# Kernel tuning notes

Measured on AMD Instinct MI355X. Metric: run time of the kernel, lower is better.

## Reference

```python
import jax, jax.numpy as jnp
import numpy as np
from jax import lax

B, H, W, CIN = 32, 64, 64, 128
F, KH, KW = 256, 3, 3
NCLS = 10


def setup_inputs() -> dict:
    key = jax.random.key(0)
    k1, k2, k3, k4 = jax.random.split(key, 4)
    x = jax.random.normal(k1, (B, H, W, CIN), dtype=jnp.float32)
    classes = jax.random.randint(k2, (B, 1), 0, NCLS, dtype=jnp.int32)
    kernel = jax.random.normal(k3, (NCLS, KH, KW, CIN, F), dtype=jnp.float32) * 0.05
    bias = jax.random.normal(k4, (NCLS, F), dtype=jnp.float32) * 0.05
    return {"x": x, "classes": classes, "kernel": kernel, "bias": bias}


def reference(x, classes, kernel, bias):
    # classes: [B,1] -> [B]
    cls = jnp.squeeze(classes, axis=1)
    k_per = kernel[cls]   # [B, KH, KW, CIN, F] per-sample gathered expert kernel
    b_per = bias[cls]     # [B, F]

    def conv_one(xi, ki):
        # xi: [H,W,CIN], ki: [KH,KW,CIN,F]
        y = lax.conv_general_dilated(
            xi[None], ki,
            window_strides=(1, 1),
            padding="SAME",
            rhs_dilation=(1, 1),
            dimension_numbers=("NHWC", "HWIO", "NHWC"),
        )
        return y[0]

    out = jax.vmap(conv_one)(x, k_per)          # [B,H,W,F]
    out = out + b_per[:, None, None, :]
    return out
```

## Files before the change

kernel.cpp:

```cpp
#include <hip/hip_runtime.h>
#include <stdint.h>

#define BATCH 32
#define CINX 128
#define FOUT 256
#define NCLS 10
#define NSTEP 18

typedef __bf16 bf16x8 __attribute__((ext_vector_type(8)));
typedef float f32x4 __attribute__((ext_vector_type(4)));

#define WT_SLAB 32768
#define WT_BYTES ((size_t)NCLS * 9 * WT_SLAB * 2)
#define Z_BYTES 4096
#define X16_BYTES ((size_t)BATCH * 4096 * CINX * 2)
#define WS_NEED (WT_BYTES + Z_BYTES + X16_BYTES)

#define BAR() __builtin_amdgcn_s_barrier()
#define SCHEDBAR() __builtin_amdgcn_sched_barrier(0)
#define VMW4() asm volatile("s_waitcnt vmcnt(4)" ::: "memory")
#define VMW0() asm volatile("s_waitcnt vmcnt(0)" ::: "memory")

__device__ __forceinline__ void gl16(const __bf16* g, __bf16* l) {
    __builtin_amdgcn_global_load_lds(
        (const __attribute__((address_space(1))) void*)g,
        (__attribute__((address_space(3))) void*)l, 16, 0, 0);
}

__global__ __launch_bounds__(256) void prep_all(const float* __restrict__ kin,
                                                __bf16* __restrict__ wt,
                                                const float* __restrict__ x,
                                                __bf16* __restrict__ x16,
                                                __bf16* __restrict__ zbuf) {
    if (blockIdx.x < NCLS * 9) {
        __shared__ __bf16 tile[128 * 260];
        const int slab = blockIdx.x;
        const float* src = kin + (size_t)slab * (CINX * FOUT);
        __bf16* dst = wt + (size_t)slab * WT_SLAB;
        const int t = threadIdx.x;
#pragma unroll
        for (int i = 0; i < 32; ++i) {
            int e4 = t + i * 256;
            int c = e4 >> 6, f4 = e4 & 63;
            f32x4 v = *(const f32x4*)(src + (size_t)e4 * 4);
            __bf16* p = &tile[c * 260 + f4 * 4];
            p[0] = (__bf16)v[0]; p[1] = (__bf16)v[1];
            p[2] = (__bf16)v[2]; p[3] = (__bf16)v[3];
        }
        __syncthreads();
#pragma unroll
        for (int i = 0; i < 16; ++i) {
            int g = t + i * 256;
            int h = g >> 10;
            int u = g & 1023;
            int f = u >> 2, slot = u & 3;
            int cu = slot ^ ((f >> 1) & 3);
            int c0 = h * 32 + cu * 8;
            bf16x8 o;
#pragma unroll
            for (int j = 0; j < 8; ++j) o[j] = tile[(c0 + j) * 260 + f];
            *(bf16x8*)(dst + (size_t)g * 8) = o;
        }
    } else {
        const int bx = blockIdx.x - NCLS * 9;
        const size_t u = (size_t)bx * 256 + threadIdx.x;
        f32x4 a = *(const f32x4*)(x + u * 8);
        f32x4 c = *(const f32x4*)(x + u * 8 + 4);
        bf16x8 o;
#pragma unroll
        for (int j = 0; j < 4; ++j) { o[j] = (__bf16)a[j]; o[4 + j] = (__bf16)c[j]; }
        *(bf16x8*)(x16 + u * 8) = o;
        if (bx == 0 && threadIdx.x < 128) {
            bf16x8 z;
#pragma unroll
            for (int j = 0; j < 8; ++j) z[j] = (__bf16)0.f;
            *(bf16x8*)(zbuf + (size_t)threadIdx.x * 8) = z;
        }
    }
}

__global__ __launch_bounds__(512, 2) void conv_main8(
    const __bf16* __restrict__ xg16, const int* __restrict__ cls_g,
    const __bf16* __restrict__ wt, const float* __restrict__ bias,
    const __bf16* __restrict__ zbuf, float* __restrict__ out) {
    __shared__ __align__(16) __bf16 ldsA[2][2][1024 * 8];
    __shared__ __align__(16) __bf16 ldsB[2][2][1024 * 8];

    const int bid0 = blockIdx.x;
    const int swz  = (bid0 & 7) * 64 + (bid0 >> 3);
    const int b    = swz >> 4;
    const int pt   = swz & 15;
    const int cls  = cls_g[b];
    const int y0   = pt << 2;

    const int tid  = threadIdx.x;
    const int lane = tid & 63;
    const int wid  = tid >> 6;
    const int wm   = wid >> 2;
    const int wn   = wid & 3;
    const int l15  = lane & 15;
    const int l4   = lane >> 4;

    const __bf16* xb   = xg16 + (size_t)b * 4096 * CINX;
    const __bf16* wcls = wt + (size_t)cls * 9 * WT_SLAB;

    int pyA[2], gxA[2], cuoffA[2], uS[2];
#pragma unroll
    for (int i = 0; i < 2; ++i) {
        int u = i * 512 + tid;
        int px = u >> 2, slot = u & 3;
        uS[i] = u;
        pyA[i] = px >> 6;
        gxA[i] = px & 63;
        cuoffA[i] = (slot ^ ((px >> 1) & 3)) * 8;
    }
    int unA[8], unB[4];
#pragma unroll
    for (int mt = 0; mt < 8; ++mt) {
        int px = wm * 128 + mt * 16 + l15;
        unA[mt] = px * 4 + (l4 ^ ((px >> 1) & 3));
    }
#pragma unroll
    for (int nt = 0; nt < 4; ++nt) {
        int f = wn * 64 + nt * 16 + l15;
        unB[nt] = f * 4 + (l4 ^ ((f >> 1) & 3));
    }

    f32x4 acc[8][4];
#pragma unroll
    for (int i = 0; i < 8; ++i)
#pragma unroll
        for (int j = 0; j < 4; ++j)
#pragma unroll
            for (int r = 0; r < 4; ++r) acc[i][j][r] = 0.f;

    auto stage = [&](int s2, int kk) {
        const int p = s2 & 1;
        const int tap = s2 >> 1;
        const int dy = tap / 3 - 1, dx = tap % 3 - 1;
        const int choff = (s2 & 1) * 64 + kk * 32;
#pragma unroll
        for (int i = 0; i < 2; ++i) {
            const int gy = y0 + pyA[i] + dy;
            const int gx = gxA[i] + dx;
            const bool v = ((unsigned)gy < 64u) && ((unsigned)gx < 64u);
            const __bf16* src = v
                ? (xb + ((size_t)(gy * 64 + gx)) * CINX + choff + cuoffA[i])
                : (zbuf + (size_t)(uS[i] & 63) * 8);
            gl16(src, &ldsA[p][kk][(size_t)uS[i] * 8]);
        }
        const __bf16* wsrc = wcls + (size_t)tap * WT_SLAB +
                             (size_t)((s2 & 1) * 2 + kk) * 8192;
#pragma unroll
        for (int i = 0; i < 2; ++i)
            gl16(wsrc + (size_t)uS[i] * 8, &ldsB[p][kk][(size_t)uS[i] * 8]);
    };

    bf16x8 afr[4], bfr[4];
    auto ldB = [&](int p, int kk) {
#pragma unroll
        for (int nt = 0; nt < 4; ++nt)
            bfr[nt] = *(const bf16x8*)&ldsB[p][kk][(size_t)unB[nt] * 8];
    };
    auto ldA = [&](int p, int kk, int mh) {
#pragma unroll
        for (int mt = 0; mt < 4; ++mt)
            afr[mt] = *(const bf16x8*)&ldsA[p][kk][(size_t)unA[mh * 4 + mt] * 8];
    };
    auto mm = [&](int mh) {
        __builtin_amdgcn_s_setprio(1);
#pragma unroll
        for (int mt = 0; mt < 4; ++mt)
#pragma unroll
            for (int nt = 0; nt < 4; ++nt)
                acc[mh * 4 + mt][nt] = __builtin_amdgcn_mfma_f32_16x16x32_bf16(
                    afr[mt], bfr[nt], acc[mh * 4 + mt][nt], 0, 0, 0);
        __builtin_amdgcn_s_setprio(0);
    };

    stage(0, 0);
    stage(0, 1);
    VMW4();
    BAR();
    SCHEDBAR();

    for (int s = 0; s < NSTEP - 1; ++s) {
        const int p = s & 1;
        ldB(p, 0); ldA(p, 0, 0); stage(s + 1, 0);
        mm(0);
        ldA(p, 0, 1);
        VMW4();
        BAR();
        SCHEDBAR();
        mm(1);
        ldB(p, 1); ldA(p, 1, 0); stage(s + 1, 1);
        mm(0);
        ldA(p, 1, 1);
        VMW4();
        BAR();
        SCHEDBAR();
        mm(1);
    }
    ldB(1, 0); ldA(1, 0, 0);
    mm(0);
    ldA(1, 0, 1);
    VMW0();
    BAR();
    SCHEDBAR();
    mm(1);
    ldB(1, 1); ldA(1, 1, 0);
    mm(0);
    ldA(1, 1, 1);
    mm(1);

    float bv[4];
#pragma unroll
    for (int nt = 0; nt < 4; ++nt)
        bv[nt] = bias[cls * FOUT + wn * 64 + nt * 16 + l15];

    float* ob = out + ((size_t)b * 4096 + (size_t)pt * 256) * FOUT;
#pragma unroll
    for (int mt = 0; mt < 8; ++mt) {
#pragma unroll
        for (int r = 0; r < 4; ++r) {
            const int row = wm * 128 + mt * 16 + l4 * 4 + r;
            float* orow = ob + (size_t)row * FOUT;
#pragma unroll
            for (int nt = 0; nt < 4; ++nt)
                orow[wn * 64 + nt * 16 + l15] = acc[mt][nt][r] + bv[nt];
        }
    }
}

__global__ __launch_bounds__(256) void prep_w_fb(const float* __restrict__ kin,
                                                 __bf16* __restrict__ wt) {
    __shared__ __bf16 tile[128 * 260];
    const int slab = blockIdx.x;
    const float* src = kin + (size_t)slab * (CINX * FOUT);
    __bf16* dst = wt + (size_t)slab * (16 * 256 * 8);
    const int t = threadIdx.x;
#pragma unroll
    for (int i = 0; i < 32; ++i) {
        int e4 = t + i * 256;
        int c = e4 >> 6, f4 = e4 & 63;
        f32x4 v = *(const f32x4*)(src + (size_t)e4 * 4);
        __bf16* p = &tile[c * 260 + f4 * 4];
        p[0] = (__bf16)v[0]; p[1] = (__bf16)v[1];
        p[2] = (__bf16)v[2]; p[3] = (__bf16)v[3];
    }
    __syncthreads();
#pragma unroll
    for (int i = 0; i < 16; ++i) {
        int g = t + i * 256;
        int cu = g >> 8, f = g & 255;
        bf16x8 o;
#pragma unroll
        for (int j = 0; j < 8; ++j) o[j] = tile[(cu * 8 + j) * 260 + f];
        *(bf16x8*)(dst + (size_t)g * 8) = o;
    }
}

__global__ __launch_bounds__(512, 2) void conv_fb(
    const float* __restrict__ xg, const int* __restrict__ cls_g,
    const __bf16* __restrict__ wt, const float* __restrict__ bias,
    float* __restrict__ out) {
    __shared__ __align__(16) __bf16 ldsA[2][8 * 256 * 8];
    __shared__ __align__(16) __bf16 ldsB[2][8 * 256 * 8];
    const int bid0 = blockIdx.x;
    const int swz = (bid0 & 7) * 64 + (bid0 >> 3);
    const int b = swz >> 4, pt = swz & 15;
    const int cls = cls_g[b];
    const int y0 = pt << 2;
    const int tid = threadIdx.x, lane = tid & 63, wid = tid >> 6;
    const int wm = wid >> 2, wn = wid & 3, l15 = lane & 15, l4 = lane >> 4;
    const float* xb = xg + (size_t)b * 4096 * CINX;
    const __bf16* wcls = wt + (size_t)cls * 9 * (16 * 256 * 8);
    const int tpx = tid >> 1, tch = (tid & 1) * 32;
    const int py = tpx >> 6, px_ = tpx & 63;
    f32x4 acc[8][4];
#pragma unroll
    for (int i = 0; i < 8; ++i)
#pragma unroll
        for (int j = 0; j < 4; ++j)
#pragma unroll
            for (int r = 0; r < 4; ++r) acc[i][j][r] = 0.f;
    f32x4 va[8];
    auto issueB = [&](int s, int buf) {
        const int tap = s >> 1, chalf = (s & 1) << 6;
        const __bf16* wsrc = wcls + (size_t)tap * (16 * 256 * 8) + chalf * 256;
#pragma unroll
        for (int i = 0; i < 4; ++i) {
            const int u = i * 512 + tid;
            gl16(wsrc + (size_t)u * 8, &ldsB[buf][(size_t)u * 8]);
        }
    };
    auto issueA = [&](int s) {
        const int tap = s >> 1, chalf = (s & 1) << 6;
        const int dy = tap / 3 - 1, dx = tap % 3 - 1;
        const int gy = y0 + py + dy, gx = px_ + dx;
        const bool valid = ((unsigned)gy < 64u) && ((unsigned)gx < 64u);
        const float* src = xb + ((size_t)(gy * 64 + gx)) * CINX + chalf + tch;
        if (valid) {
#pragma unroll
            for (int j2 = 0; j2 < 8; ++j2) va[j2] = *(const f32x4*)(src + j2 * 4);
        } else {
#pragma unroll
            for (int j2 = 0; j2 < 8; ++j2)
#pragma unroll
                for (int q = 0; q < 4; ++q) va[j2][q] = 0.f;
        }
    };
    auto writeA = [&](int buf) {
#pragma unroll
        for (int j = 0; j < 4; ++j) {
            bf16x8 pk;
#pragma unroll
            for (int q = 0; q < 4; ++q) {
                pk[q] = (__bf16)va[2 * j][q];
                pk[4 + q] = (__bf16)va[2 * j + 1][q];
            }
            const int u = ((tid & 1) * 4 + j) * 256 + tpx;
            *(bf16x8*)(&ldsA[buf][(size_t)u * 8]) = pk;
        }
    };
    auto compute = [&](int buf) {
#pragma unroll
        for (int kk = 0; kk < 2; ++kk) {
            const int cu = kk * 4 + l4;
            bf16x8 afr[8], bfr[4];
#pragma unroll
            for (int mt = 0; mt < 8; ++mt)
                afr[mt] = *(const bf16x8*)(
                    &ldsA[buf][(size_t)(cu * 256 + wm * 128 + mt * 16 + l15) * 8]);
#pragma unroll
            for (int nt = 0; nt < 4; ++nt)
                bfr[nt] = *(const bf16x8*)(
                    &ldsB[buf][(size_t)(cu * 256 + wn * 64 + nt * 16 + l15) * 8]);
#pragma unroll
            for (int mt = 0; mt < 8; ++mt)
#pragma unroll
                for (int nt = 0; nt < 4; ++nt)
                    acc[mt][nt] = __builtin_amdgcn_mfma_f32_16x16x32_bf16(
                        afr[mt], bfr[nt], acc[mt][nt], 0, 0, 0);
        }
    };
    issueB(0, 0);
    issueA(0);
    writeA(0);
    __syncthreads();
    int cur = 0;
    for (int s = 0; s < NSTEP - 1; ++s) {
        issueB(s + 1, cur ^ 1);
        issueA(s + 1);
        compute(cur);
        writeA(cur ^ 1);
        __syncthreads();
        cur ^= 1;
    }
    compute(cur);
    float bv[4];
#pragma unroll
    for (int nt = 0; nt < 4; ++nt)
        bv[nt] = bias[cls * FOUT + wn * 64 + nt * 16 + l15];
    float* ob = out + ((size_t)b * 4096 + (size_t)pt * 256) * FOUT;
#pragma unroll
    for (int mt = 0; mt < 8; ++mt) {
#pragma unroll
        for (int r = 0; r < 4; ++r) {
            const int row = wm * 128 + mt * 16 + l4 * 4 + r;
            float* orow = ob + (size_t)row * FOUT;
#pragma unroll
            for (int nt = 0; nt < 4; ++nt)
                orow[wn * 64 + nt * 16 + l15] = acc[mt][nt][r] + bv[nt];
        }
    }
}

extern "C" void kernel_launch(void* const* d_in, const int* in_sizes, int n_in,
                              void* d_out, int out_size, void* d_ws, size_t ws_size,
                              hipStream_t stream) {
    const float* x       = (const float*)d_in[0];
    const int*   classes = (const int*)d_in[1];
    const float* kin     = (const float*)d_in[2];
    const float* bias    = (const float*)d_in[3];
    float* out = (float*)d_out;

    char* ws = (char*)d_ws;
    __bf16* wt   = (__bf16*)ws;
    __bf16* zbuf = (__bf16*)(ws + WT_BYTES);
    __bf16* x16  = (__bf16*)(ws + WT_BYTES + Z_BYTES);

    if (ws_size >= WS_NEED) {
        prep_all<<<dim3(NCLS * 9 + 8192), dim3(256), 0, stream>>>(kin, wt, x,
                                                                  x16, zbuf);
        conv_main8<<<dim3(512), dim3(512), 0, stream>>>(x16, classes, wt, bias,
                                                        zbuf, out);
    } else {
        prep_w_fb<<<dim3(NCLS * 9), dim3(256), 0, stream>>>(kin, wt);
        conv_fb<<<dim3(512), dim3(512), 0, stream>>>(x, classes, wt, bias, out);
    }
}
```

Measured before the change: 101.7 us.

## Split conv tiles over output features and shrink LDS for higher occupancy

The main conv kernel now gives each block half of the 256 output features, so there are 1024 blocks, each with a 256x128 tile and 4x4 accumulators per wave instead of 8x4. LDS staging is cut to a 32-channel slice per step, double-buffered over 36 steps, and launch bounds request 4 blocks per CU. The aim is more resident waves to hide load latency and a better spread across CUs. The cost is that every input pixel tile is loaded twice (once per feature half), the pipeline has more, shorter steps and more barriers, and each wave gets less data reuse.

```diff
diff --git a/kernel.cpp b/kernel.cpp
--- a/kernel.cpp
+++ b/kernel.cpp
@@ -5,7 +5,7 @@
 #define CINX 128
 #define FOUT 256
 #define NCLS 10
-#define NSTEP 18
+#define NSTEP36 36
 
 typedef __bf16 bf16x8 __attribute__((ext_vector_type(8)));
 typedef float f32x4 __attribute__((ext_vector_type(4)));
@@ -18,7 +18,8 @@
 
 #define BAR() __builtin_amdgcn_s_barrier()
 #define SCHEDBAR() __builtin_amdgcn_sched_barrier(0)
-#define VMW4() asm volatile("s_waitcnt vmcnt(4)" ::: "memory")
+#define LGKM0() asm volatile("s_waitcnt lgkmcnt(0)" ::: "memory")
+#define VMW3() asm volatile("s_waitcnt vmcnt(3)" ::: "memory")
 #define VMW0() asm volatile("s_waitcnt vmcnt(0)" ::: "memory")
 
 __device__ __forceinline__ void gl16(const __bf16* g, __bf16* l) {
@@ -51,11 +52,11 @@
 #pragma unroll
         for (int i = 0; i < 16; ++i) {
             int g = t + i * 256;
-            int h = g >> 10;
+            int c32 = g >> 10;
             int u = g & 1023;
             int f = u >> 2, slot = u & 3;
             int cu = slot ^ ((f >> 1) & 3);
-            int c0 = h * 32 + cu * 8;
+            int c0 = c32 * 32 + cu * 8;
             bf16x8 o;
 #pragma unroll
             for (int j = 0; j < 8; ++j) o[j] = tile[(c0 + j) * 260 + f];
@@ -79,151 +80,140 @@
     }
 }
 
-__global__ __launch_bounds__(512, 2) void conv_main8(
+__global__ __launch_bounds__(512, 4) void conv_hi(
     const __bf16* __restrict__ xg16, const int* __restrict__ cls_g,
     const __bf16* __restrict__ wt, const float* __restrict__ bias,
     const __bf16* __restrict__ zbuf, float* __restrict__ out) {
-    __shared__ __align__(16) __bf16 ldsA[2][2][1024 * 8];
-    __shared__ __align__(16) __bf16 ldsB[2][2][1024 * 8];
+    __shared__ __align__(16) __bf16 ldsA[2][256 * 32];
+    __shared__ __align__(16) __bf16 ldsB[2][128 * 32];
 
     const int bid0 = blockIdx.x;
-    const int swz  = (bid0 & 7) * 64 + (bid0 >> 3);
-    const int b    = swz >> 4;
-    const int pt   = swz & 15;
+    const int swz  = (bid0 & 7) * 128 + (bid0 >> 3);
+    const int b    = swz >> 5;
+    const int pt   = (swz >> 1) & 15;
+    const int ft   = swz & 1;
     const int cls  = cls_g[b];
     const int y0   = pt << 2;
 
     const int tid  = threadIdx.x;
     const int lane = tid & 63;
     const int wid  = tid >> 6;
-    const int wm   = wid >> 2;
-    const int wn   = wid & 3;
+    const int wm   = wid >> 1;
+    const int wn   = wid & 1;
     const int l15  = lane & 15;
     const int l4   = lane >> 4;
 
     const __bf16* xb   = xg16 + (size_t)b * 4096 * CINX;
     const __bf16* wcls = wt + (size_t)cls * 9 * WT_SLAB;
 
-    int pyA[2], gxA[2], cuoffA[2], uS[2];
+    int pyA[2], gxA[2], cuoffA[2];
 #pragma unroll
     for (int i = 0; i < 2; ++i) {
         int u = i * 512 + tid;
         int px = u >> 2, slot = u & 3;
-        uS[i] = u;
         pyA[i] = px >> 6;
         gxA[i] = px & 63;
         cuoffA[i] = (slot ^ ((px >> 1) & 3)) * 8;
     }
-    int unA[8], unB[4];
-#pragma unroll
-    for (int mt = 0; mt < 8; ++mt) {
-        int px = wm * 128 + mt * 16 + l15;
-        unA[mt] = px * 4 + (l4 ^ ((px >> 1) & 3));
-    }
-#pragma unroll
-    for (int nt = 0; nt < 4; ++nt) {
-        int f = wn * 64 + nt * 16 + l15;
-        unB[nt] = f * 4 + (l4 ^ ((f >> 1) & 3));
-    }
-
-    f32x4 acc[8][4];
-#pragma unroll
-    for (int i = 0; i < 8; ++i)
+    const int swq = (l15 >> 1) & 3;
+    int unA[4], unB[4];
+#pragma unroll
+    for (int mt = 0; mt < 4; ++mt)
+        unA[mt] = (wm * 64 + mt * 16 + l15) * 4 + (l4 ^ swq);
+#pragma unroll
+    for (int nt = 0; nt < 4; ++nt)
+        unB[nt] = (wn * 64 + nt * 16 + l15) * 4 + (l4 ^ swq);
+
+    f32x4 acc[4][4];
+#pragma unroll
+    for (int i = 0; i < 4; ++i)
 #pragma unroll
         for (int j = 0; j < 4; ++j)
 #pragma unroll
             for (int r = 0; r < 4; ++r) acc[i][j][r] = 0.f;
 
-    auto stage = [&](int s2, int kk) {
-        const int p = s2 & 1;
-        const int tap = s2 >> 1;
+    auto stage = [&](int s2, int buf) {
+        const int tap = s2 >> 2, c32 = s2 & 3;
         const int dy = tap / 3 - 1, dx = tap % 3 - 1;
-        const int choff = (s2 & 1) * 64 + kk * 32;
+        const int choff = c32 * 32;
 #pragma unroll
         for (int i = 0; i < 2; ++i) {
+            const int u = i * 512 + tid;
             const int gy = y0 + pyA[i] + dy;
             const int gx = gxA[i] + dx;
             const bool v = ((unsigned)gy < 64u) && ((unsigned)gx < 64u);
             const __bf16* src = v
                 ? (xb + ((size_t)(gy * 64 + gx)) * CINX + choff + cuoffA[i])
-                : (zbuf + (size_t)(uS[i] & 63) * 8);
-            gl16(src, &ldsA[p][kk][(size_t)uS[i] * 8]);
+                : (zbuf + (size_t)(u & 63) * 8);
+            gl16(src, &ldsA[buf][(size_t)u * 8]);
         }
         const __bf16* wsrc = wcls + (size_t)tap * WT_SLAB +
-                             (size_t)((s2 & 1) * 2 + kk) * 8192;
-#pragma unroll
-        for (int i = 0; i < 2; ++i)
-            gl16(wsrc + (size_t)uS[i] * 8, &ldsB[p][kk][(size_t)uS[i] * 8]);
+                             (size_t)(c32 * 1024 + ft * 512 + tid) * 8;
+        gl16(wsrc, &ldsB[buf][(size_t)tid * 8]);
     };
 
     bf16x8 afr[4], bfr[4];
-    auto ldB = [&](int p, int kk) {
+    auto rdfrags = [&](int buf) {
+#pragma unroll
+        for (int mt = 0; mt < 4; ++mt)
+            afr[mt] = *(const bf16x8*)&ldsA[buf][(size_t)unA[mt] * 8];
 #pragma unroll
         for (int nt = 0; nt < 4; ++nt)
-            bfr[nt] = *(const bf16x8*)&ldsB[p][kk][(size_t)unB[nt] * 8];
-    };
-    auto ldA = [&](int p, int kk, int mh) {
+            bfr[nt] = *(const bf16x8*)&ldsB[buf][(size_t)unB[nt] * 8];
+    };
+    auto mm = [&]() {
+        __builtin_amdgcn_s_setprio(1);
 #pragma unroll
         for (int mt = 0; mt < 4; ++mt)
-            afr[mt] = *(const bf16x8*)&ldsA[p][kk][(size_t)unA[mh * 4 + mt] * 8];
-    };
-    auto mm = [&](int mh) {
-        __builtin_amdgcn_s_setprio(1);
-#pragma unroll
-        for (int mt = 0; mt < 4; ++mt)
 #pragma unroll
             for (int nt = 0; nt < 4; ++nt)
-                acc[mh * 4 + mt][nt] = __builtin_amdgcn_mfma_f32_16x16x32_bf16(
-                    afr[mt], bfr[nt], acc[mh * 4 + mt][nt], 0, 0, 0);
+                acc[mt][nt] = __builtin_amdgcn_mfma_f32_16x16x32_bf16(
+                    afr[mt], bfr[nt], acc[mt][nt], 0, 0, 0);
         __builtin_amdgcn_s_setprio(0);
     };
 
     stage(0, 0);
-    stage(0, 1);
-    VMW4();
+    stage(1, 1);
+    VMW3();
     BAR();
+
+    for (int s = 0; s < NSTEP36 - 2; s += 2) {
+#pragma unroll
+        for (int half = 0; half < 2; ++half) {
+            const int buf = half;
+            rdfrags(buf);
+            LGKM0();
+            SCHEDBAR();
+            BAR();
+            stage(s + half + 2, buf);
+            mm();
+            VMW3();
+            BAR();
+        }
+    }
+    rdfrags(0);
+    LGKM0();
     SCHEDBAR();
-
-    for (int s = 0; s < NSTEP - 1; ++s) {
-        const int p = s & 1;
-        ldB(p, 0); ldA(p, 0, 0); stage(s + 1, 0);
-        mm(0);
-        ldA(p, 0, 1);
-        VMW4();
-        BAR();
-        SCHEDBAR();
-        mm(1);
-        ldB(p, 1); ldA(p, 1, 0); stage(s + 1, 1);
-        mm(0);
-        ldA(p, 1, 1);
-        VMW4();
-        BAR();
-        SCHEDBAR();
-        mm(1);
-    }
-    ldB(1, 0); ldA(1, 0, 0);
-    mm(0);
-    ldA(1, 0, 1);
+    BAR();
+    mm();
     VMW0();
     BAR();
+    rdfrags(1);
+    LGKM0();
     SCHEDBAR();
-    mm(1);
-    ldB(1, 1); ldA(1, 1, 0);
-    mm(0);
-    ldA(1, 1, 1);
-    mm(1);
+    mm();
 
     float bv[4];
 #pragma unroll
     for (int nt = 0; nt < 4; ++nt)
-        bv[nt] = bias[cls * FOUT + wn * 64 + nt * 16 + l15];
-
-    float* ob = out + ((size_t)b * 4096 + (size_t)pt * 256) * FOUT;
-#pragma unroll
-    for (int mt = 0; mt < 8; ++mt) {
+        bv[nt] = bias[cls * FOUT + ft * 128 + wn * 64 + nt * 16 + l15];
+
+    float* ob = out + ((size_t)b * 4096 + (size_t)pt * 256) * FOUT + ft * 128;
+#pragma unroll
+    for (int mt = 0; mt < 4; ++mt) {
 #pragma unroll
         for (int r = 0; r < 4; ++r) {
-            const int row = wm * 128 + mt * 16 + l4 * 4 + r;
+            const int row = wm * 64 + mt * 16 + l4 * 4 + r;
             float* orow = ob + (size_t)row * FOUT;
 #pragma unroll
             for (int nt = 0; nt < 4; ++nt)
@@ -349,7 +339,7 @@
     writeA(0);
     __syncthreads();
     int cur = 0;
-    for (int s = 0; s < NSTEP - 1; ++s) {
+    for (int s = 0; s < 17; ++s) {
         issueB(s + 1, cur ^ 1);
         issueA(s + 1);
         compute(cur);
@@ -393,8 +383,8 @@
     if (ws_size >= WS_NEED) {
         prep_all<<<dim3(NCLS * 9 + 8192), dim3(256), 0, stream>>>(kin, wt, x,
                                                                   x16, zbuf);
-        conv_main8<<<dim3(512), dim3(512), 0, stream>>>(x16, classes, wt, bias,
-                                                        zbuf, out);
+        conv_hi<<<dim3(1024), dim3(512), 0, stream>>>(x16, classes, wt, bias,
+                                                      zbuf, out);
     } else {
         prep_w_fb<<<dim3(NCLS * 9), dim3(256), 0, stream>>>(kin, wt);
         conv_fb<<<dim3(512), dim3(512), 0, stream>>>(x, classes, wt, bias, out);
```

Result: slower. 104.4 us (+2.6%).

## Switch conv main loop to 32x32x16 MFMA with double-buffered register fragments

Applied to the files above, without the earlier changes.

Replaces the 16x16x32 bf16 MFMA tiling with 32x32x16 tiles (4x2 per wave instead of 8x4), so fewer LDS fragment reads are needed per FLOP. It adds ping-pong register fragment sets so LDS reads for the next k-step overlap the current MFMAs. It also precomputes per-thread source pointers and a per-tap validity bitmask to cut address arithmetic in the staging loop, and fully unrolls the main loop. The risks are higher register pressure under the 2-blocks-per-SM launch bound, and a more complex output row mapping.

```diff
diff --git a/kernel.cpp b/kernel.cpp
--- a/kernel.cpp
+++ b/kernel.cpp
@@ -5,10 +5,10 @@
 #define CINX 128
 #define FOUT 256
 #define NCLS 10
-#define NSTEP 18
 
 typedef __bf16 bf16x8 __attribute__((ext_vector_type(8)));
 typedef float f32x4 __attribute__((ext_vector_type(4)));
+typedef float f32x16 __attribute__((ext_vector_type(16)));
 
 #define WT_SLAB 32768
 #define WT_BYTES ((size_t)NCLS * 9 * WT_SLAB * 2)
@@ -21,7 +21,7 @@
 #define VMW4() asm volatile("s_waitcnt vmcnt(4)" ::: "memory")
 #define VMW0() asm volatile("s_waitcnt vmcnt(0)" ::: "memory")
 
-__device__ __forceinline__ void gl16(const __bf16* g, __bf16* l) {
+__device__ __forceinline__ void gl16(const void* g, void* l) {
     __builtin_amdgcn_global_load_lds(
         (const __attribute__((address_space(1))) void*)g,
         (__attribute__((address_space(3))) void*)l, 16, 0, 0);
@@ -51,11 +51,11 @@
 #pragma unroll
         for (int i = 0; i < 16; ++i) {
             int g = t + i * 256;
-            int h = g >> 10;
+            int c32 = g >> 10;
             int u = g & 1023;
             int f = u >> 2, slot = u & 3;
             int cu = slot ^ ((f >> 1) & 3);
-            int c0 = h * 32 + cu * 8;
+            int c0 = c32 * 32 + cu * 8;
             bf16x8 o;
 #pragma unroll
             for (int j = 0; j < 8; ++j) o[j] = tile[(c0 + j) * 260 + f];
@@ -79,12 +79,11 @@
     }
 }
 
-__global__ __launch_bounds__(512, 2) void conv_main8(
+__global__ __launch_bounds__(512, 2) void conv32(
     const __bf16* __restrict__ xg16, const int* __restrict__ cls_g,
     const __bf16* __restrict__ wt, const float* __restrict__ bias,
     const __bf16* __restrict__ zbuf, float* __restrict__ out) {
-    __shared__ __align__(16) __bf16 ldsA[2][2][1024 * 8];
-    __shared__ __align__(16) __bf16 ldsB[2][2][1024 * 8];
+    __shared__ __align__(16) char lds[131072];
 
     const int bid0 = blockIdx.x;
     const int swz  = (bid0 & 7) * 64 + (bid0 >> 3);
@@ -98,83 +97,99 @@
     const int wid  = tid >> 6;
     const int wm   = wid >> 2;
     const int wn   = wid & 3;
-    const int l15  = lane & 15;
-    const int l4   = lane >> 4;
+    const int l31  = lane & 31;
+    const int hi   = lane >> 5;
 
     const __bf16* xb   = xg16 + (size_t)b * 4096 * CINX;
     const __bf16* wcls = wt + (size_t)cls * 9 * WT_SLAB;
 
-    int pyA[2], gxA[2], cuoffA[2], uS[2];
+    const __bf16* PA[2];
+    const __bf16* WB[2];
+    const __bf16* ZS[2];
+    int vmask[2];
+    int dstu[2];
 #pragma unroll
     for (int i = 0; i < 2; ++i) {
-        int u = i * 512 + tid;
-        int px = u >> 2, slot = u & 3;
-        uS[i] = u;
-        pyA[i] = px >> 6;
-        gxA[i] = px & 63;
-        cuoffA[i] = (slot ^ ((px >> 1) & 3)) * 8;
-    }
-    int unA[8], unB[4];
-#pragma unroll
-    for (int mt = 0; mt < 8; ++mt) {
-        int px = wm * 128 + mt * 16 + l15;
-        unA[mt] = px * 4 + (l4 ^ ((px >> 1) & 3));
-    }
-#pragma unroll
-    for (int nt = 0; nt < 4; ++nt) {
-        int f = wn * 64 + nt * 16 + l15;
-        unB[nt] = f * 4 + (l4 ^ ((f >> 1) & 3));
-    }
-
-    f32x4 acc[8][4];
-#pragma unroll
-    for (int i = 0; i < 8; ++i)
-#pragma unroll
-        for (int j = 0; j < 4; ++j)
-#pragma unroll
-            for (int r = 0; r < 4; ++r) acc[i][j][r] = 0.f;
+        const int u = i * 512 + tid;
+        const int px = u >> 2, slot = u & 3;
+        const int py = px >> 6, gx = px & 63;
+        const int cuoff = (slot ^ ((px >> 1) & 3)) * 8;
+        const int ay = y0 + py;
+        PA[i] = xb + ((size_t)(ay * 64 + gx)) * CINX + cuoff;
+        WB[i] = wcls + (size_t)u * 8;
+        ZS[i] = zbuf + (size_t)(u & 63) * 8;
+        dstu[i] = u * 16;
+        int m = 0;
+#pragma unroll
+        for (int tap = 0; tap < 9; ++tap) {
+            const int dy = tap / 3 - 1, dx = tap % 3 - 1;
+            const int yy = ay + dy, xx = gx + dx;
+            if (true) m |= ((((unsigned)yy < 64u) && ((unsigned)xx < 64u)) ? 1 : 0) << tap;
+        }
+        vmask[i] = m;
+    }
+
+    int adA[2][4], adB[2][2];
+#pragma unroll
+    for (int mt = 0; mt < 4; ++mt) {
+        const int px = wm * 128 + mt * 32 + l31;
+        const int sw = (px >> 1) & 3;
+#pragma unroll
+        for (int ks = 0; ks < 2; ++ks)
+            adA[ks][mt] = (px * 4 + ((2 * ks + hi) ^ sw)) * 16;
+    }
+#pragma unroll
+    for (int nt = 0; nt < 2; ++nt) {
+        const int f = wn * 64 + nt * 32 + l31;
+        const int sw = (f >> 1) & 3;
+#pragma unroll
+        for (int ks = 0; ks < 2; ++ks)
+            adB[ks][nt] = 65536 + (f * 4 + ((2 * ks + hi) ^ sw)) * 16;
+    }
+
+    f32x16 acc[4][2];
+#pragma unroll
+    for (int i = 0; i < 4; ++i)
+#pragma unroll
+        for (int j = 0; j < 2; ++j)
+#pragma unroll
+            for (int r = 0; r < 16; ++r) acc[i][j][r] = 0.f;
 
     auto stage = [&](int s2, int kk) {
-        const int p = s2 & 1;
+        const int pk  = (s2 & 1) * 2 + kk;
         const int tap = s2 >> 1;
         const int dy = tap / 3 - 1, dx = tap % 3 - 1;
-        const int choff = (s2 & 1) * 64 + kk * 32;
+        const int cq = (s2 & 1) * 2 + kk;
+        const int aoff = (dy * 64 + dx) * CINX + cq * 32;
+        const size_t woff = (size_t)tap * WT_SLAB + (size_t)cq * 8192;
 #pragma unroll
         for (int i = 0; i < 2; ++i) {
-            const int gy = y0 + pyA[i] + dy;
-            const int gx = gxA[i] + dx;
-            const bool v = ((unsigned)gy < 64u) && ((unsigned)gx < 64u);
-            const __bf16* src = v
-                ? (xb + ((size_t)(gy * 64 + gx)) * CINX + choff + cuoffA[i])
-                : (zbuf + (size_t)(uS[i] & 63) * 8);
-            gl16(src, &ldsA[p][kk][(size_t)uS[i] * 8]);
-        }
-        const __bf16* wsrc = wcls + (size_t)tap * WT_SLAB +
-                             (size_t)((s2 & 1) * 2 + kk) * 8192;
+            const __bf16* src = ((vmask[i] >> tap) & 1) ? (PA[i] + aoff) : ZS[i];
+            gl16(src, lds + pk * 16384 + dstu[i]);
+        }
 #pragma unroll
         for (int i = 0; i < 2; ++i)
-            gl16(wsrc + (size_t)uS[i] * 8, &ldsB[p][kk][(size_t)uS[i] * 8]);
-    };
-
-    bf16x8 afr[4], bfr[4];
-    auto ldB = [&](int p, int kk) {
-#pragma unroll
-        for (int nt = 0; nt < 4; ++nt)
-            bfr[nt] = *(const bf16x8*)&ldsB[p][kk][(size_t)unB[nt] * 8];
-    };
-    auto ldA = [&](int p, int kk, int mh) {
+            gl16(WB[i] + woff, lds + 65536 + pk * 16384 + dstu[i]);
+    };
+
+    bf16x8 AS[2][4], BS[2][2];
+    auto rd = [&](int set, int pk, int ks) {
+        const int off = pk * 16384;
 #pragma unroll
         for (int mt = 0; mt < 4; ++mt)
-            afr[mt] = *(const bf16x8*)&ldsA[p][kk][(size_t)unA[mh * 4 + mt] * 8];
-    };
-    auto mm = [&](int mh) {
+            AS[set][mt] = *(const bf16x8*)(lds + off + adA[ks][mt]);
+#pragma unroll
+        for (int nt = 0; nt < 2; ++nt)
+            BS[set][nt] = *(const bf16x8*)(lds + off + adB[ks][nt]);
+    };
+    auto mm = [&](int set) {
         __builtin_amdgcn_s_setprio(1);
 #pragma unroll
         for (int mt = 0; mt < 4; ++mt)
 #pragma unroll
-            for (int nt = 0; nt < 4; ++nt)
-                acc[mh * 4 + mt][nt] = __builtin_amdgcn_mfma_f32_16x16x32_bf16(
-                    afr[mt], bfr[nt], acc[mh * 4 + mt][nt], 0, 0, 0);
+            for (int nt = 0; nt < 2; ++nt)
+                acc[mt][nt] = __builtin_amdgcn_mfma_f32_32x32x16_bf16(
+                    AS[set][mt], BS[set][nt], acc[mt][nt], 0, 0, 0);
         __builtin_amdgcn_s_setprio(0);
     };
 
@@ -183,51 +198,56 @@
     VMW4();
     BAR();
     SCHEDBAR();
-
-    for (int s = 0; s < NSTEP - 1; ++s) {
-        const int p = s & 1;
-        ldB(p, 0); ldA(p, 0, 0); stage(s + 1, 0);
+    rd(0, 0, 0);
+
+#pragma unroll
+    for (int s = 0; s < 17; ++s) {
+        const int pk0 = (s & 1) * 2;
+        const int pk1 = pk0 + 1;
+        const int pkn = ((s + 1) & 1) * 2;
+        rd(1, pk0, 1);
+        stage(s + 1, 0);
         mm(0);
-        ldA(p, 0, 1);
         VMW4();
         BAR();
         SCHEDBAR();
+        rd(0, pk1, 0);
         mm(1);
-        ldB(p, 1); ldA(p, 1, 0); stage(s + 1, 1);
+        rd(1, pk1, 1);
+        stage(s + 1, 1);
         mm(0);
-        ldA(p, 1, 1);
         VMW4();
         BAR();
         SCHEDBAR();
+        rd(0, pkn, 0);
         mm(1);
     }
-    ldB(1, 0); ldA(1, 0, 0);
+    rd(1, 2, 1);
     mm(0);
-    ldA(1, 0, 1);
     VMW0();
     BAR();
     SCHEDBAR();
+    rd(0, 3, 0);
     mm(1);
-    ldB(1, 1); ldA(1, 1, 0);
+    rd(1, 3, 1);
     mm(0);
-    ldA(1, 1, 1);
     mm(1);
 
-    float bv[4];
-#pragma unroll
-    for (int nt = 0; nt < 4; ++nt)
-        bv[nt] = bias[cls * FOUT + wn * 64 + nt * 16 + l15];
+    float bv[2];
+#pragma unroll
+    for (int nt = 0; nt < 2; ++nt)
+        bv[nt] = bias[cls * FOUT + wn * 64 + nt * 32 + l31];
 
     float* ob = out + ((size_t)b * 4096 + (size_t)pt * 256) * FOUT;
 #pragma unroll
-    for (int mt = 0; mt < 8; ++mt) {
-#pragma unroll
-        for (int r = 0; r < 4; ++r) {
-            const int row = wm * 128 + mt * 16 + l4 * 4 + r;
+    for (int mt = 0; mt < 4; ++mt) {
+#pragma unroll
+        for (int r = 0; r < 16; ++r) {
+            const int row = wm * 128 + mt * 32 + (r & 3) + 8 * (r >> 2) + 4 * hi;
             float* orow = ob + (size_t)row * FOUT;
 #pragma unroll
-            for (int nt = 0; nt < 4; ++nt)
-                orow[wn * 64 + nt * 16 + l15] = acc[mt][nt][r] + bv[nt];
+            for (int nt = 0; nt < 2; ++nt)
+                orow[wn * 64 + nt * 32 + l31] = acc[mt][nt][r] + bv[nt];
         }
     }
 }
@@ -349,7 +369,7 @@
     writeA(0);
     __syncthreads();
     int cur = 0;
-    for (int s = 0; s < NSTEP - 1; ++s) {
+    for (int s = 0; s < 17; ++s) {
         issueB(s + 1, cur ^ 1);
         issueA(s + 1);
         compute(cur);
@@ -393,8 +413,8 @@
     if (ws_size >= WS_NEED) {
         prep_all<<<dim3(NCLS * 9 + 8192), dim3(256), 0, stream>>>(kin, wt, x,
                                                                   x16, zbuf);
-        conv_main8<<<dim3(512), dim3(512), 0, stream>>>(x16, classes, wt, bias,
-                                                        zbuf, out);
+        conv32<<<dim3(512), dim3(512), 0, stream>>>(x16, classes, wt, bias,
+                                                    zbuf, out);
     } else {
         prep_w_fb<<<dim3(NCLS * 9), dim3(256), 0, stream>>>(kin, wt);
         conv_fb<<<dim3(512), dim3(512), 0, stream>>>(x, classes, wt, bias, out);
```

After: 107.4 us. 5.6% more time.

## Stage halo input tile once per channel chunk and reuse across all nine taps

Applied to the files above, without the earlier changes.

The conv kernel now loads a 6x66 halo region of the input into LDS once per 32-channel chunk and reads all nine shifted taps from it. Previously it re-gathered shifted input pixels from global memory for every tap. The loop is also reordered to tap-inner/channel-outer over 36 steps, with a 4-deep ring of weight buffers and barriers only at chunk boundaries. This cuts global and L2 traffic for activations and shortens each step's sync pattern, but it uses a single A buffer, so the halo reload stalls at each chunk boundary, and the larger LDS footprint (96KB) may limit occupancy.

```diff
diff --git a/kernel.cpp b/kernel.cpp
--- a/kernel.cpp
+++ b/kernel.cpp
@@ -5,7 +5,6 @@
 #define CINX 128
 #define FOUT 256
 #define NCLS 10
-#define NSTEP 18
 
 typedef __bf16 bf16x8 __attribute__((ext_vector_type(8)));
 typedef float f32x4 __attribute__((ext_vector_type(4)));
@@ -18,10 +17,12 @@
 
 #define BAR() __builtin_amdgcn_s_barrier()
 #define SCHEDBAR() __builtin_amdgcn_sched_barrier(0)
-#define VMW4() asm volatile("s_waitcnt vmcnt(4)" ::: "memory")
+#define LGKM0() asm volatile("s_waitcnt lgkmcnt(0)" ::: "memory")
+#define VMW6() asm volatile("s_waitcnt vmcnt(6)" ::: "memory")
+#define VMW2() asm volatile("s_waitcnt vmcnt(2)" ::: "memory")
 #define VMW0() asm volatile("s_waitcnt vmcnt(0)" ::: "memory")
 
-__device__ __forceinline__ void gl16(const __bf16* g, __bf16* l) {
+__device__ __forceinline__ void gl16(const void* g, void* l) {
     __builtin_amdgcn_global_load_lds(
         (const __attribute__((address_space(1))) void*)g,
         (__attribute__((address_space(3))) void*)l, 16, 0, 0);
@@ -51,11 +52,11 @@
 #pragma unroll
         for (int i = 0; i < 16; ++i) {
             int g = t + i * 256;
-            int h = g >> 10;
+            int c32 = g >> 10;
             int u = g & 1023;
             int f = u >> 2, slot = u & 3;
             int cu = slot ^ ((f >> 1) & 3);
-            int c0 = h * 32 + cu * 8;
+            int c0 = c32 * 32 + cu * 8;
             bf16x8 o;
 #pragma unroll
             for (int j = 0; j < 8; ++j) o[j] = tile[(c0 + j) * 260 + f];
@@ -79,12 +80,11 @@
     }
 }
 
-__global__ __launch_bounds__(512, 2) void conv_main8(
+__global__ __launch_bounds__(512, 2) void conv_halo(
     const __bf16* __restrict__ xg16, const int* __restrict__ cls_g,
     const __bf16* __restrict__ wt, const float* __restrict__ bias,
     const __bf16* __restrict__ zbuf, float* __restrict__ out) {
-    __shared__ __align__(16) __bf16 ldsA[2][2][1024 * 8];
-    __shared__ __align__(16) __bf16 ldsB[2][2][1024 * 8];
+    __shared__ __align__(16) char lds[98304];
 
     const int bid0 = blockIdx.x;
     const int swz  = (bid0 & 7) * 64 + (bid0 >> 3);
@@ -103,27 +103,53 @@
 
     const __bf16* xb   = xg16 + (size_t)b * 4096 * CINX;
     const __bf16* wcls = wt + (size_t)cls * 9 * WT_SLAB;
-
-    int pyA[2], gxA[2], cuoffA[2], uS[2];
-#pragma unroll
-    for (int i = 0; i < 2; ++i) {
-        int u = i * 512 + tid;
-        int px = u >> 2, slot = u & 3;
-        uS[i] = u;
-        pyA[i] = px >> 6;
-        gxA[i] = px & 63;
-        cuoffA[i] = (slot ^ ((px >> 1) & 3)) * 8;
-    }
-    int unA[8], unB[4];
+    const char*   ZS   = (const char*)zbuf + (tid & 255) * 16;
+
+    const __bf16* PAH[4];
+    bool okJ[4];
+#pragma unroll
+    for (int j = 0; j < 4; ++j) {
+        const int q = j * 512 + tid;
+        const int hpx = q >> 2, slot = q & 3;
+        const int row = hpx / 66;
+        const int col = hpx - row * 66;
+        const int y = y0 + row - 1, xc = col - 1;
+        const bool ok = (hpx < 396) && ((unsigned)y < 64u) && ((unsigned)xc < 64u);
+        const int chunk = slot ^ ((hpx >> 1) & 3);
+        const int yy = ok ? y : 0, xx = ok ? xc : 0;
+        PAH[j] = xb + ((size_t)(yy * 64 + xx)) * CINX + chunk * 8;
+        okJ[j] = ok;
+    }
+    auto stageA = [&](int cq2) {
+#pragma unroll
+        for (int j = 0; j < 4; ++j) {
+            const void* src = okJ[j] ? (const void*)(PAH[j] + cq2 * 32)
+                                     : (const void*)ZS;
+            gl16(src, lds + (j * 512 + tid) * 16);
+        }
+    };
+    auto stageB = [&](int s2) {
+        const int tap2 = s2 % 9, cq2 = s2 / 9;
+        const __bf16* wsrc = wcls + (size_t)tap2 * WT_SLAB + cq2 * 8192;
+        char* dst = lds + 32768 + (s2 & 3) * 16384;
+#pragma unroll
+        for (int i = 0; i < 2; ++i) {
+            const int q = i * 512 + tid;
+            gl16(wsrc + (size_t)q * 8, dst + q * 16);
+        }
+    };
+
+    int hpx0[8];
 #pragma unroll
     for (int mt = 0; mt < 8; ++mt) {
-        int px = wm * 128 + mt * 16 + l15;
-        unA[mt] = px * 4 + (l4 ^ ((px >> 1) & 3));
-    }
+        const int px = wm * 128 + mt * 16 + l15;
+        hpx0[mt] = ((px >> 6) + 1) * 66 + (px & 63) + 1;
+    }
+    int adB[4];
 #pragma unroll
     for (int nt = 0; nt < 4; ++nt) {
-        int f = wn * 64 + nt * 16 + l15;
-        unB[nt] = f * 4 + (l4 ^ ((f >> 1) & 3));
+        const int f = wn * 64 + nt * 16 + l15;
+        adB[nt] = (f * 4 + (l4 ^ ((f >> 1) & 3))) * 16;
     }
 
     f32x4 acc[8][4];
@@ -134,84 +160,81 @@
 #pragma unroll
             for (int r = 0; r < 4; ++r) acc[i][j][r] = 0.f;
 
-    auto stage = [&](int s2, int kk) {
-        const int p = s2 & 1;
-        const int tap = s2 >> 1;
-        const int dy = tap / 3 - 1, dx = tap % 3 - 1;
-        const int choff = (s2 & 1) * 64 + kk * 32;
-#pragma unroll
-        for (int i = 0; i < 2; ++i) {
-            const int gy = y0 + pyA[i] + dy;
-            const int gx = gxA[i] + dx;
-            const bool v = ((unsigned)gy < 64u) && ((unsigned)gx < 64u);
-            const __bf16* src = v
-                ? (xb + ((size_t)(gy * 64 + gx)) * CINX + choff + cuoffA[i])
-                : (zbuf + (size_t)(uS[i] & 63) * 8);
-            gl16(src, &ldsA[p][kk][(size_t)uS[i] * 8]);
-        }
-        const __bf16* wsrc = wcls + (size_t)tap * WT_SLAB +
-                             (size_t)((s2 & 1) * 2 + kk) * 8192;
-#pragma unroll
-        for (int i = 0; i < 2; ++i)
-            gl16(wsrc + (size_t)uS[i] * 8, &ldsB[p][kk][(size_t)uS[i] * 8]);
-    };
-
-    bf16x8 afr[4], bfr[4];
-    auto ldB = [&](int p, int kk) {
-#pragma unroll
-        for (int nt = 0; nt < 4; ++nt)
-            bfr[nt] = *(const bf16x8*)&ldsB[p][kk][(size_t)unB[nt] * 8];
-    };
-    auto ldA = [&](int p, int kk, int mh) {
-#pragma unroll
-        for (int mt = 0; mt < 4; ++mt)
-            afr[mt] = *(const bf16x8*)&ldsA[p][kk][(size_t)unA[mh * 4 + mt] * 8];
-    };
-    auto mm = [&](int mh) {
-        __builtin_amdgcn_s_setprio(1);
-#pragma unroll
-        for (int mt = 0; mt < 4; ++mt)
-#pragma unroll
-            for (int nt = 0; nt < 4; ++nt)
-                acc[mh * 4 + mt][nt] = __builtin_amdgcn_mfma_f32_16x16x32_bf16(
-                    afr[mt], bfr[nt], acc[mh * 4 + mt][nt], 0, 0, 0);
-        __builtin_amdgcn_s_setprio(0);
-    };
-
-    stage(0, 0);
-    stage(0, 1);
-    VMW4();
+    stageA(0);
+    stageB(0);
+    stageB(1);
+    VMW2();
     BAR();
     SCHEDBAR();
 
-    for (int s = 0; s < NSTEP - 1; ++s) {
-        const int p = s & 1;
-        ldB(p, 0); ldA(p, 0, 0); stage(s + 1, 0);
-        mm(0);
-        ldA(p, 0, 1);
-        VMW4();
-        BAR();
-        SCHEDBAR();
-        mm(1);
-        ldB(p, 1); ldA(p, 1, 0); stage(s + 1, 1);
-        mm(0);
-        ldA(p, 1, 1);
-        VMW4();
-        BAR();
-        SCHEDBAR();
-        mm(1);
-    }
-    ldB(1, 0); ldA(1, 0, 0);
-    mm(0);
-    ldA(1, 0, 1);
-    VMW0();
-    BAR();
-    SCHEDBAR();
-    mm(1);
-    ldB(1, 1); ldA(1, 1, 0);
-    mm(0);
-    ldA(1, 1, 1);
-    mm(1);
+#pragma unroll
+    for (int s = 0; s < 36; ++s) {
+        const int tap = s % 9, cq = s / 9;
+        const int dy = tap / 3 - 1, dx = tap % 3 - 1;
+        const int D = dy * 66 + dx;
+        const bool bound = (tap == 8) && (cq < 3);
+        const bool postb = (tap == 0) && (cq > 0);
+
+        if (postb) {
+            VMW2();
+            BAR();
+            SCHEDBAR();
+        }
+
+        const char* bb = lds + 32768 + (s & 3) * 16384;
+        bf16x8 BF[4], AF0[4], AF1[4];
+#pragma unroll
+        for (int nt = 0; nt < 4; ++nt)
+            BF[nt] = *(const bf16x8*)(bb + adB[nt]);
+        auto lda = [&](int mt) {
+            const int h = hpx0[mt] + D;
+            const int sl = l4 ^ ((h >> 1) & 3);
+            return *(const bf16x8*)(lds + h * 64 + sl * 16);
+        };
+#pragma unroll
+        for (int mt = 0; mt < 4; ++mt) AF0[mt] = lda(mt);
+
+        if (bound) {
+#pragma unroll
+            for (int mt = 0; mt < 4; ++mt) AF1[mt] = lda(mt + 4);
+            LGKM0();
+            SCHEDBAR();
+            BAR();
+            stageA(cq + 1);
+            if (s < 34) stageB(s + 2);
+        } else {
+            if (s < 34) stageB(s + 2);
+#pragma unroll
+            for (int mt = 0; mt < 4; ++mt) AF1[mt] = lda(mt + 4);
+        }
+
+        __builtin_amdgcn_s_setprio(1);
+#pragma unroll
+        for (int mt = 0; mt < 4; ++mt)
+#pragma unroll
+            for (int nt = 0; nt < 4; ++nt)
+                acc[mt][nt] = __builtin_amdgcn_mfma_f32_16x16x32_bf16(
+                    AF0[mt], BF[nt], acc[mt][nt], 0, 0, 0);
+#pragma unroll
+        for (int mt = 0; mt < 4; ++mt)
+#pragma unroll
+            for (int nt = 0; nt < 4; ++nt)
+                acc[mt + 4][nt] = __builtin_amdgcn_mfma_f32_16x16x32_bf16(
+                    AF1[mt], BF[nt], acc[mt + 4][nt], 0, 0, 0);
+        __builtin_amdgcn_s_setprio(0);
+
+        if (bound) {
+            VMW6();
+        } else if (s < 34) {
+            VMW2();
+        } else if (s == 34) {
+            VMW0();
+        }
+        if (s < 35) {
+            BAR();
+            SCHEDBAR();
+        }
+    }
 
     float bv[4];
 #pragma unroll
@@ -349,7 +372,7 @@
     writeA(0);
     __syncthreads();
     int cur = 0;
-    for (int s = 0; s < NSTEP - 1; ++s) {
+    for (int s = 0; s < 17; ++s) {
         issueB(s + 1, cur ^ 1);
         issueA(s + 1);
         compute(cur);
@@ -393,8 +416,8 @@
     if (ws_size >= WS_NEED) {
         prep_all<<<dim3(NCLS * 9 + 8192), dim3(256), 0, stream>>>(kin, wt, x,
                                                                   x16, zbuf);
-        conv_main8<<<dim3(512), dim3(512), 0, stream>>>(x16, classes, wt, bias,
-                                                        zbuf, out);
+        conv_halo<<<dim3(512), dim3(512), 0, stream>>>(x16, classes, wt, bias,
+                                                       zbuf, out);
     } else {
         prep_w_fb<<<dim3(NCLS * 9), dim3(256), 0, stream>>>(kin, wt);
         conv_fb<<<dim3(512), dim3(512), 0, stream>>>(x, classes, wt, bias, out);
```

Result: slower. 125.9 us (+23.8%).
